# Kernel optimization log

Hardware: AMD Instinct MI355X
Metric: run time of the kernel (lower is better)

The kernel has to match this reference:

```python
import jax, jax.numpy as jnp
import numpy as np

B, N, E = 2, 20000, 160000
D, U = 1, 100          # input_dim, num_units
IN = D + U             # 101
NEG_SLOPE = 0.2        # PyG GATv2Conv default


def setup_inputs() -> dict:
    key = jax.random.key(0)
    ks = jax.random.split(key, 20)
    s = 0.1
    inp = {
        "inputs": jax.random.normal(ks[0], (B, N * D), jnp.float32),
        "state": jax.random.normal(ks[1], (B, N * U), jnp.float32),
        "src": jax.random.randint(ks[2], (E,), 0, N),
        "dst": jax.random.randint(ks[3], (E,), 0, N),
        # GATv2Conv(101, 200) params: lin_l, lin_r, att, out-bias
        "Wl1": jax.random.normal(ks[4], (IN, 2 * U), jnp.float32) * s,
        "bl1": jax.random.normal(ks[5], (2 * U,), jnp.float32) * s,
        "Wr1": jax.random.normal(ks[6], (IN, 2 * U), jnp.float32) * s,
        "br1": jax.random.normal(ks[7], (2 * U,), jnp.float32) * s,
        "att1": jax.random.normal(ks[8], (2 * U,), jnp.float32) * s,
        "bg1": jax.random.normal(ks[9], (2 * U,), jnp.float32) * s,
        "bias0": jax.random.normal(ks[10], (2 * U,), jnp.float32) * s,
        # GATv2Conv(101, 100) params
        "Wl2": jax.random.normal(ks[11], (IN, U), jnp.float32) * s,
        "bl2": jax.random.normal(ks[12], (U,), jnp.float32) * s,
        "Wr2": jax.random.normal(ks[13], (IN, U), jnp.float32) * s,
        "br2": jax.random.normal(ks[14], (U,), jnp.float32) * s,
        "att2": jax.random.normal(ks[15], (U,), jnp.float32) * s,
        "bg2": jax.random.normal(ks[16], (U,), jnp.float32) * s,
        "bias1": jax.random.normal(ks[17], (U,), jnp.float32) * s,
    }
    return inp


def _gatv2(x, src_f, dst_f, Wl, bl, Wr, br, att, bg):
    # x: (B, N, IN); edges (with self-loops) flow src -> dst.
    xl = x @ Wl + bl                                   # (B, N, C) source transform
    xr = x @ Wr + br                                   # (B, N, C) target transform
    msg = jax.nn.leaky_relu(xl[:, src_f] + xr[:, dst_f], NEG_SLOPE)  # (B, Ef, C)
    e = jnp.einsum('bec,c->be', msg, att)              # (B, Ef) attention logits
    seg_max = jax.vmap(lambda v: jax.ops.segment_max(v, dst_f, num_segments=N))(e)
    ea = jnp.exp(e - seg_max[:, dst_f])
    denom = jax.vmap(lambda v: jax.ops.segment_sum(v, dst_f, num_segments=N))(ea)
    alpha = ea / denom[:, dst_f]                       # per-target softmax
    out = jax.vmap(
        lambda a, xs: jax.ops.segment_sum(a[:, None] * xs, dst_f, num_segments=N)
    )(alpha, xl[:, src_f])                             # (B, N, C)
    return out + bg


def reference(inputs, state, src, dst,
              Wl1, bl1, Wr1, br1, att1, bg1, bias0,
              Wl2, bl2, Wr2, br2, att2, bg2, bias1):
    loops = jnp.arange(N)
    src_f = jnp.concatenate([src, loops])              # PyG adds self-loops
    dst_f = jnp.concatenate([dst, loops])
    inputs3 = inputs.reshape(B, N, D)
    state3 = state.reshape(B, N, U)

    # _gc1: GATv2(101 -> 200) + bias_0, sigmoid gates r, u
    xs = jnp.concatenate([inputs3, state3], axis=2)    # (B, N, 101)
    g1 = _gatv2(xs, src_f, dst_f, Wl1, bl1, Wr1, br1, att1, bg1) + bias0
    val = jax.nn.sigmoid(g1)                           # (B, N, 200)
    r = val[..., :U].reshape(B, N * U)
    u = val[..., U:].reshape(B, N * U)

    # _gc2: GATv2(101 -> 100) on [inputs, r*state] + bias_1, tanh
    xs2 = jnp.concatenate([inputs3, (r * state).reshape(B, N, U)], axis=2)
    c = jnp.tanh(_gatv2(xs2, src_f, dst_f, Wl2, bl2, Wr2, br2, att2, bg2) + bias1)
    c = c.reshape(B, N * U)

    new_state = u * state + (1.0 - u) * c              # (B, N*U)
    return new_state
```

## Files before the change

kernel.cpp:

```cpp
#include <hip/hip_runtime.h>
#include <stdint.h>

typedef __attribute__((ext_vector_type(8))) short short8;
typedef __attribute__((ext_vector_type(4))) short short4v;
typedef __attribute__((ext_vector_type(4))) float f32x4;
typedef __attribute__((ext_vector_type(2))) float f32x2;

static constexpr int BB = 2, NN = 20000, UU = 100;
static constexpr int C1 = 200, C2 = 100;
static constexpr int MT = BB * NN;
static constexpr int MPAD = 40064;
static constexpr float NEG = 0.2f;
static constexpr float THR = 20.f;

__device__ __forceinline__ float b2f(short s) {
  union { uint32_t u; float f; } cv; cv.u = ((uint32_t)(uint16_t)s) << 16; return cv.f;
}
__device__ __forceinline__ short f2b(float x) {
  union { float f; uint32_t u; } cv; cv.f = x;
  uint32_t r = cv.u + 0x7FFFu + ((cv.u >> 16) & 1u);
  return (short)(r >> 16);
}
__device__ __forceinline__ int swz(int r, int e) {
  return (((e >> 3) ^ (r & 7)) << 3) + (e & 7);
}
__device__ __forceinline__ int ilv(int m) {
  return (m < NN) ? 2 * m : 2 * (m - NN) + 1;
}

#define GL2LDS(gsrc, ldst)                                                          \
  __builtin_amdgcn_global_load_lds((const __attribute__((address_space(1))) void*)(gsrc), \
                                   (__attribute__((address_space(3))) void*)(ldst), 16, 0, 0)


__global__ void k_zero(int* __restrict__ p, int n) {
  int i = blockIdx.x * 256 + threadIdx.x;
  if (i < n) p[i] = 0;
}

__global__ void k_hist(const int* __restrict__ dst, int E, int* __restrict__ hist) {
  int e = blockIdx.x * 256 + threadIdx.x;
  if (e < E) atomicAdd(&hist[dst[e]], 1);
}

__global__ __launch_bounds__(1024) void k_scan(int* __restrict__ histcur,
                                               int* __restrict__ rowptr, int N, int E) {
  __shared__ int part[1024];
  int t = threadIdx.x;
  int CH = (N + 1023) / 1024;
  int beg = t * CH; if (beg > N) beg = N;
  int end = beg + CH; if (end > N) end = N;
  int s = 0;
  for (int i = beg; i < end; ++i) s += histcur[i];
  part[t] = s;
  __syncthreads();
  for (int off = 1; off < 1024; off <<= 1) {
    int v = (t >= off) ? part[t - off] : 0;
    __syncthreads();
    part[t] += v;
    __syncthreads();
  }
  int base = (t == 0) ? 0 : part[t - 1];
  for (int i = beg; i < end; ++i) {
    int h = histcur[i];
    rowptr[i] = base;
    histcur[i] = base;
    base += h;
  }
  if (t == 1023) rowptr[N] = part[1023];
}

__global__ void k_scatter(const int* __restrict__ src, const int* __restrict__ dst, int E,
                          int* __restrict__ cursor, int* __restrict__ col) {
  int e = blockIdx.x * 256 + threadIdx.x;
  if (e < E) {
    int p = atomicAdd(&cursor[dst[e]], 1);
    col[p] = src[e];
  }
}


__global__ void k_buildA1(const float* __restrict__ inp, const float* __restrict__ st,
                          short* __restrict__ A) {
  int t = blockIdx.x * 256 + threadIdx.x;
  if (t >= MT * 16) return;
  int r = t >> 4, g = t & 15;
  short8 v;
#pragma unroll
  for (int j = 0; j < 8; ++j) {
    int e = g * 8 + j;
    float x = 0.f;
    if (e == 0) x = inp[r];
    else if (e <= 100) x = st[(size_t)r * 100 + e - 1];
    v[j] = f2b(x);
  }
  *(short8*)(A + (size_t)r * 128 + (((g ^ (r & 7)) << 3))) = v;
}

__global__ void k_buildBT(const float* __restrict__ Wl, const float* __restrict__ Wr,
                          short* __restrict__ BT, int SPLIT, int NPAD, int rot) {
  int t = blockIdx.x * 256 + threadIdx.x;
  if (t >= NPAD * 16) return;
  int n = t >> 4, g = t & 15;
  short8 v;
#pragma unroll
  for (int j = 0; j < 8; ++j) {
    int k = g * 8 + j;
    int ksrc = rot ? (k < 100 ? k + 1 : (k == 100 ? 0 : -1)) : (k < 101 ? k : -1);
    float x = 0.f;
    if (ksrc >= 0 && n < 2 * SPLIT)
      x = (n < SPLIT) ? Wl[(size_t)ksrc * SPLIT + n] : Wr[(size_t)ksrc * SPLIT + n - SPLIT];
    v[j] = f2b(x);
  }
  *(short8*)(BT + (size_t)n * 128 + ((g ^ (n & 7)) << 3)) = v;
}

__global__ void k_fillA2(const float* __restrict__ inp, short* __restrict__ A) {
  int r = blockIdx.x * 256 + threadIdx.x;
  if (r >= MT) return;
  short* row = A + (size_t)r * 128;
  row[swz(r, 100)] = f2b(inp[r]);
#pragma unroll
  for (int e = 101; e < 128; ++e) row[swz(r, e)] = 0;
}


template<int NOUT, int SPLIT>
__global__ __launch_bounds__(256) void k_gemm(
    const short* __restrict__ A, const short* __restrict__ BT,
    const float* __restrict__ bias_l, const float* __restrict__ bias_r,
    short* __restrict__ X) {
  __shared__ __align__(16) short As[128 * 128];
  __shared__ __align__(16) short Bs[128 * 128];
  int tid = threadIdx.x;
  int m0 = blockIdx.x * 128;
  int n0 = blockIdx.y * 128;
  {
    const short* gA = A + (size_t)m0 * 128;
    const short* gB = BT + (size_t)n0 * 128;
#pragma unroll
    for (int i = 0; i < 8; ++i) {
      GL2LDS(gA + i * 2048 + tid * 8, As + i * 2048 + tid * 8);
      GL2LDS(gB + i * 2048 + tid * 8, Bs + i * 2048 + tid * 8);
    }
  }
  __syncthreads();

  int wv = tid >> 6, lane = tid & 63;
  int m_off = (wv & 1) * 64, n_off = (wv >> 1) * 64;
  int lrow = lane & 15, lk = lane >> 4;
  f32x4 acc[4][4];
#pragma unroll
  for (int i = 0; i < 4; ++i)
#pragma unroll
    for (int j = 0; j < 4; ++j) acc[i][j] = (f32x4){0.f, 0.f, 0.f, 0.f};

#pragma unroll
  for (int kk = 0; kk < 4; ++kk) {
    int g = kk * 4 + lk;
    short8 a[4], b[4];
#pragma unroll
    for (int f = 0; f < 4; ++f) {
      int ra = m_off + f * 16 + lrow;
      a[f] = *(const short8*)(As + ra * 128 + ((g ^ (ra & 7)) << 3));
      int rb = n_off + f * 16 + lrow;
      b[f] = *(const short8*)(Bs + rb * 128 + ((g ^ (rb & 7)) << 3));
    }
#pragma unroll
    for (int i = 0; i < 4; ++i)
#pragma unroll
      for (int j = 0; j < 4; ++j)
        acc[i][j] = __builtin_amdgcn_mfma_f32_16x16x32_bf16(a[i], b[j], acc[i][j], 0, 0, 0);
  }

#pragma unroll
  for (int j = 0; j < 4; ++j) {
    int n = n0 + n_off + j * 16 + lrow;
    bool nok = n < NOUT;
    float bv = 0.f;
    if (nok) bv = (n < SPLIT) ? bias_l[n] : bias_r[n - SPLIT];
#pragma unroll
    for (int i = 0; i < 4; ++i) {
      int mb = m0 + m_off + i * 16 + lk * 4;
#pragma unroll
      for (int r = 0; r < 4; ++r) {
        int m = mb + r;
        if (nok && m < MT) X[(size_t)ilv(m) * NOUT + n] = f2b(acc[i][j][r] + bv);
      }
    }
  }
}


__global__ __launch_bounds__(256) void k_agg1(
    const short* __restrict__ X1, const int* __restrict__ rowptr, const int* __restrict__ col,
    const float* __restrict__ att, const float* __restrict__ bgv, const float* __restrict__ bias0,
    const float* __restrict__ st, short* __restrict__ A2, float* __restrict__ uu) {
  int w = threadIdx.x >> 6, lane = threadIdx.x & 63;
  int n = blockIdx.x * 4 + w;
  if (n >= NN) return;
  int half = lane >> 5, ll = lane & 31;
  int c0 = (ll < 25 ? ll : 24) * 8;
  int idx = half * NN + n;
  const short* xb = X1 + (size_t)half * 400 + c0;

  float attv[8], xrv[8], num[8];
  {
    f32x4 a0 = (f32x4){0,0,0,0}, a1 = (f32x4){0,0,0,0};
    if (ll < 25) { a0 = *(const f32x4*)(att + c0); a1 = *(const f32x4*)(att + c0 + 4); }
#pragma unroll
    for (int q = 0; q < 4; ++q) { attv[q] = a0[q]; attv[4 + q] = a1[q]; }
    short8 xr8 = *(const short8*)(X1 + (size_t)(2 * n + half) * 400 + 200 + c0);
#pragma unroll
    for (int q = 0; q < 8; ++q) xrv[q] = (ll < 25) ? b2f(xr8[q]) : 0.f;
  }
  float m, denom = 1.f;
  {
    short8 v = *(const short8*)(xb + (size_t)(2 * n) * 400);
    float e = 0.f;
#pragma unroll
    for (int q = 0; q < 8; ++q) {
      float x = b2f(v[q]);
      num[q] = x;
      float msg = x + xrv[q];
      msg = (msg > 0.f) ? msg : NEG * msg;
      e = fmaf(msg, attv[q], e);
    }
#pragma unroll
    for (int off = 16; off > 0; off >>= 1) e += __shfl_xor(e, off);
    m = e;
  }

  int beg = rowptr[n], end = rowptr[n + 1];
  for (int base = beg; base < end; base += 64) {
    int cnt = min(end - base, 64);
    int cv = col[base + (lane < cnt ? lane : 0)];
    int p = 0;
    for (; p + 2 <= cnt; p += 2) {
      int s0 = __shfl(cv, p), s1 = __shfl(cv, p + 1);
      short8 v0 = *(const short8*)(xb + (size_t)(2 * s0) * 400);
      short8 v1 = *(const short8*)(xb + (size_t)(2 * s1) * 400);
      float xs0[8], xs1[8];
      float e0 = 0.f, e1 = 0.f;
#pragma unroll
      for (int q = 0; q < 8; ++q) {
        xs0[q] = b2f(v0[q]);
        float m0_ = xs0[q] + xrv[q]; m0_ = (m0_ > 0.f) ? m0_ : NEG * m0_;
        e0 = fmaf(m0_, attv[q], e0);
        xs1[q] = b2f(v1[q]);
        float m1_ = xs1[q] + xrv[q]; m1_ = (m1_ > 0.f) ? m1_ : NEG * m1_;
        e1 = fmaf(m1_, attv[q], e1);
      }
#pragma unroll
      for (int off = 16; off > 0; off >>= 1) {
        e0 += __shfl_xor(e0, off);
        e1 += __shfl_xor(e1, off);
      }
      float d0 = e0 - m;
      if (d0 > THR) {
        float so = __expf(-d0); denom *= so;
#pragma unroll
        for (int q = 0; q < 8; ++q) num[q] *= so;
        m = e0; d0 = 0.f;
      }
      float pe0 = __expf(d0);
      denom += pe0;
#pragma unroll
      for (int q = 0; q < 8; ++q) num[q] = fmaf(pe0, xs0[q], num[q]);
      float d1 = e1 - m;
      if (d1 > THR) {
        float so = __expf(-d1); denom *= so;
#pragma unroll
        for (int q = 0; q < 8; ++q) num[q] *= so;
        m = e1; d1 = 0.f;
      }
      float pe1 = __expf(d1);
      denom += pe1;
#pragma unroll
      for (int q = 0; q < 8; ++q) num[q] = fmaf(pe1, xs1[q], num[q]);
    }
    if (p < cnt) {
      int s0 = __shfl(cv, p);
      short8 v0 = *(const short8*)(xb + (size_t)(2 * s0) * 400);
      float xs0[8];
      float e0 = 0.f;
#pragma unroll
      for (int q = 0; q < 8; ++q) {
        xs0[q] = b2f(v0[q]);
        float m0_ = xs0[q] + xrv[q]; m0_ = (m0_ > 0.f) ? m0_ : NEG * m0_;
        e0 = fmaf(m0_, attv[q], e0);
      }
#pragma unroll
      for (int off = 16; off > 0; off >>= 1) e0 += __shfl_xor(e0, off);
      float d0 = e0 - m;
      if (d0 > THR) {
        float so = __expf(-d0); denom *= so;
#pragma unroll
        for (int q = 0; q < 8; ++q) num[q] *= so;
        m = e0; d0 = 0.f;
      }
      float pe0 = __expf(d0);
      denom += pe0;
#pragma unroll
      for (int q = 0; q < 8; ++q) num[q] = fmaf(pe0, xs0[q], num[q]);
    }
  }

  float invd = 1.f / denom;
  if (ll < 25) {
    f32x4 g0 = *(const f32x4*)(bgv + c0),   g1 = *(const f32x4*)(bgv + c0 + 4);
    f32x4 h0 = *(const f32x4*)(bias0 + c0), h1 = *(const f32x4*)(bias0 + c0 + 4);
    float vq[8];
#pragma unroll
    for (int q = 0; q < 4; ++q) {
      float o0 = fmaf(num[q], invd, g0[q] + h0[q]);
      vq[q] = 1.f / (1.f + __expf(-o0));
      float o1 = fmaf(num[4 + q], invd, g1[q] + h1[q]);
      vq[4 + q] = 1.f / (1.f + __expf(-o1));
    }
    size_t sb = (size_t)idx * UU;
    if (ll < 12) {
      f32x4 s0 = *(const f32x4*)(st + sb + c0), s1 = *(const f32x4*)(st + sb + c0 + 4);
      short8 wv;
#pragma unroll
      for (int q = 0; q < 4; ++q) { wv[q] = f2b(vq[q] * s0[q]); wv[4 + q] = f2b(vq[4 + q] * s1[q]); }
      *(short8*)(A2 + (size_t)idx * 128 + ((ll ^ (idx & 7)) << 3)) = wv;
    } else if (ll == 12) {
      f32x4 s0 = *(const f32x4*)(st + sb + 96);
      short4v wv;
#pragma unroll
      for (int q = 0; q < 4; ++q) wv[q] = f2b(vq[q] * s0[q]);
      *(short4v*)(A2 + (size_t)idx * 128 + ((12 ^ (idx & 7)) << 3)) = wv;
      *(f32x4*)(uu + sb) = (f32x4){vq[4], vq[5], vq[6], vq[7]};
    } else {
      int uo = c0 - 100;
      *(f32x4*)(uu + sb + uo)     = (f32x4){vq[0], vq[1], vq[2], vq[3]};
      *(f32x4*)(uu + sb + uo + 4) = (f32x4){vq[4], vq[5], vq[6], vq[7]};
    }
  }
}

__global__ __launch_bounds__(256) void k_agg2(
    const short* __restrict__ X2, const int* __restrict__ rowptr, const int* __restrict__ col,
    const float* __restrict__ att, const float* __restrict__ bgv, const float* __restrict__ bias1,
    const float* __restrict__ st, float* __restrict__ out) {
  int w = threadIdx.x >> 6, lane = threadIdx.x & 63;
  int n = blockIdx.x * 4 + w;
  if (n >= NN) return;
  int half = lane >> 5, ll = lane & 31;
  int c0 = (ll < 25 ? ll : 24) * 4;
  int idx = half * NN + n;
  const short* xb = X2 + (size_t)half * 200 + c0;

  float attv[4], xrv[4], num[4];
  {
    f32x4 a0 = (f32x4){0,0,0,0};
    if (ll < 25) a0 = *(const f32x4*)(att + c0);
#pragma unroll
    for (int q = 0; q < 4; ++q) attv[q] = a0[q];
    short4v xr4 = *(const short4v*)(X2 + (size_t)(2 * n + half) * 200 + 100 + c0);
#pragma unroll
    for (int q = 0; q < 4; ++q) xrv[q] = (ll < 25) ? b2f(xr4[q]) : 0.f;
  }
  float m, denom = 1.f;
  {
    short4v v = *(const short4v*)(xb + (size_t)(2 * n) * 200);
    float e = 0.f;
#pragma unroll
    for (int q = 0; q < 4; ++q) {
      float x = b2f(v[q]);
      num[q] = x;
      float msg = x + xrv[q];
      msg = (msg > 0.f) ? msg : NEG * msg;
      e = fmaf(msg, attv[q], e);
    }
#pragma unroll
    for (int off = 16; off > 0; off >>= 1) e += __shfl_xor(e, off);
    m = e;
  }

  int beg = rowptr[n], end = rowptr[n + 1];
  for (int base = beg; base < end; base += 64) {
    int cnt = min(end - base, 64);
    int cv = col[base + (lane < cnt ? lane : 0)];
    int p = 0;
    for (; p + 2 <= cnt; p += 2) {
      int s0 = __shfl(cv, p), s1 = __shfl(cv, p + 1);
      short4v v0 = *(const short4v*)(xb + (size_t)(2 * s0) * 200);
      short4v v1 = *(const short4v*)(xb + (size_t)(2 * s1) * 200);
      float xs0[4], xs1[4];
      float e0 = 0.f, e1 = 0.f;
#pragma unroll
      for (int q = 0; q < 4; ++q) {
        xs0[q] = b2f(v0[q]);
        float m0_ = xs0[q] + xrv[q]; m0_ = (m0_ > 0.f) ? m0_ : NEG * m0_;
        e0 = fmaf(m0_, attv[q], e0);
        xs1[q] = b2f(v1[q]);
        float m1_ = xs1[q] + xrv[q]; m1_ = (m1_ > 0.f) ? m1_ : NEG * m1_;
        e1 = fmaf(m1_, attv[q], e1);
      }
#pragma unroll
      for (int off = 16; off > 0; off >>= 1) {
        e0 += __shfl_xor(e0, off);
        e1 += __shfl_xor(e1, off);
      }
      float d0 = e0 - m;
      if (d0 > THR) {
        float so = __expf(-d0); denom *= so;
#pragma unroll
        for (int q = 0; q < 4; ++q) num[q] *= so;
        m = e0; d0 = 0.f;
      }
      float pe0 = __expf(d0);
      denom += pe0;
#pragma unroll
      for (int q = 0; q < 4; ++q) num[q] = fmaf(pe0, xs0[q], num[q]);
      float d1 = e1 - m;
      if (d1 > THR) {
        float so = __expf(-d1); denom *= so;
#pragma unroll
        for (int q = 0; q < 4; ++q) num[q] *= so;
        m = e1; d1 = 0.f;
      }
      float pe1 = __expf(d1);
      denom += pe1;
#pragma unroll
      for (int q = 0; q < 4; ++q) num[q] = fmaf(pe1, xs1[q], num[q]);
    }
    if (p < cnt) {
      int s0 = __shfl(cv, p);
      short4v v0 = *(const short4v*)(xb + (size_t)(2 * s0) * 200);
      float xs0[4];
      float e0 = 0.f;
#pragma unroll
      for (int q = 0; q < 4; ++q) {
        xs0[q] = b2f(v0[q]);
        float m0_ = xs0[q] + xrv[q]; m0_ = (m0_ > 0.f) ? m0_ : NEG * m0_;
        e0 = fmaf(m0_, attv[q], e0);
      }
#pragma unroll
      for (int off = 16; off > 0; off >>= 1) e0 += __shfl_xor(e0, off);
      float d0 = e0 - m;
      if (d0 > THR) {
        float so = __expf(-d0); denom *= so;
#pragma unroll
        for (int q = 0; q < 4; ++q) num[q] *= so;
        m = e0; d0 = 0.f;
      }
      float pe0 = __expf(d0);
      denom += pe0;
#pragma unroll
      for (int q = 0; q < 4; ++q) num[q] = fmaf(pe0, xs0[q], num[q]);
    }
  }

  float invd = 1.f / denom;
  if (ll < 25) {
    f32x4 g0 = *(const f32x4*)(bgv + c0);
    f32x4 h0 = *(const f32x4*)(bias1 + c0);
    size_t sb = (size_t)idx * UU;
    f32x4 uv = *(const f32x4*)(out + sb + c0);
    f32x4 sv = *(const f32x4*)(st + sb + c0);
    f32x4 res;
#pragma unroll
    for (int q = 0; q < 4; ++q) {
      float o  = fmaf(num[q], invd, g0[q] + h0[q]);
      float cvh = tanhf(o);
      res[q] = uv[q] * sv[q] + (1.f - uv[q]) * cvh;
    }
    *(f32x4*)(out + sb + c0) = res;
  }
}


extern "C" void kernel_launch(void* const* d_in, const int* in_sizes, int n_in,
                              void* d_out, int out_size, void* d_ws, size_t ws_size,
                              hipStream_t stream) {
  const float* inp  = (const float*)d_in[0];
  const float* st   = (const float*)d_in[1];
  const int*   src  = (const int*)d_in[2];
  const int*   dst  = (const int*)d_in[3];
  const float* Wl1  = (const float*)d_in[4];
  const float* bl1  = (const float*)d_in[5];
  const float* Wr1  = (const float*)d_in[6];
  const float* br1  = (const float*)d_in[7];
  const float* att1 = (const float*)d_in[8];
  const float* bg1  = (const float*)d_in[9];
  const float* bias0= (const float*)d_in[10];
  const float* Wl2  = (const float*)d_in[11];
  const float* bl2  = (const float*)d_in[12];
  const float* Wr2  = (const float*)d_in[13];
  const float* br2  = (const float*)d_in[14];
  const float* att2 = (const float*)d_in[15];
  const float* bg2  = (const float*)d_in[16];
  const float* bias1= (const float*)d_in[17];

  const int N = NN;
  const int E = in_sizes[2];

  short* X1  = (short*)d_ws;
  short* X2  = X1;
  short* Aws = X1 + (size_t)MT * 400;
  short* BT1 = Aws + (size_t)MPAD * 128;
  short* BT2 = BT1 + 512 * 128;
  int* rowptr = (int*)(BT2 + 256 * 128);
  int* cursor = rowptr + (N + 1);
  int* col    = cursor + N;

  k_zero<<<(N + 255) / 256, 256, 0, stream>>>(cursor, N);
  k_hist<<<(E + 255) / 256, 256, 0, stream>>>(dst, E, cursor);
  k_scan<<<1, 1024, 0, stream>>>(cursor, rowptr, N, E);
  k_scatter<<<(E + 255) / 256, 256, 0, stream>>>(src, dst, E, cursor, col);

  k_buildA1<<<(MT * 16 + 255) / 256, 256, 0, stream>>>(inp, st, Aws);
  k_buildBT<<<(512 * 16 + 255) / 256, 256, 0, stream>>>(Wl1, Wr1, BT1, C1, 512, 0);
  k_buildBT<<<(256 * 16 + 255) / 256, 256, 0, stream>>>(Wl2, Wr2, BT2, C2, 256, 1);
  {
    dim3 g(MPAD / 128, 4);
    k_gemm<400, 200><<<g, 256, 0, stream>>>(Aws, BT1, bl1, br1, X1);
  }
  k_agg1<<<(NN + 3) / 4, 256, 0, stream>>>(X1, rowptr, col, att1, bg1, bias0, st,
                                           Aws, (float*)d_out);
  k_fillA2<<<(MT + 255) / 256, 256, 0, stream>>>(inp, Aws);
  {
    dim3 g(MPAD / 128, 2);
    k_gemm<200, 100><<<g, 256, 0, stream>>>(Aws, BT2, bl2, br2, X2);
  }
  k_agg2<<<(NN + 3) / 4, 256, 0, stream>>>(X2, rowptr, col, att2, bg2, bias1, st,
                                           (float*)d_out);
}
```

Before: 205.1 us.

## Fuse prep kernels, drop online-max softmax, unroll gathers by four, relayout X

Merges the zeroing, A1 build and both weight-transpose kernels into one prep kernel. The fillA2 kernel is folded into agg1, which now writes the input column and the zero padding itself. The GEMM output layout changes so that both batches' left features for a node sit side by side, ahead of the right features. The aggregation kernels drop the running-max rescaling in the softmax, exponentiating logits directly, and unroll the edge loop to four neighbours for more memory-level parallelism. This saves launches and branches, but relies on the logits being small enough that exp does not overflow.

```diff
diff --git a/kernel.cpp b/kernel.cpp
--- a/kernel.cpp
+++ b/kernel.cpp
@@ -4,14 +4,12 @@
 typedef __attribute__((ext_vector_type(8))) short short8;
 typedef __attribute__((ext_vector_type(4))) short short4v;
 typedef __attribute__((ext_vector_type(4))) float f32x4;
-typedef __attribute__((ext_vector_type(2))) float f32x2;
 
 static constexpr int BB = 2, NN = 20000, UU = 100;
 static constexpr int C1 = 200, C2 = 100;
 static constexpr int MT = BB * NN;
 static constexpr int MPAD = 40064;
 static constexpr float NEG = 0.2f;
-static constexpr float THR = 20.f;
 
 __device__ __forceinline__ float b2f(short s) {
   union { uint32_t u; float f; } cv; cv.u = ((uint32_t)(uint16_t)s) << 16; return cv.f;
@@ -21,22 +19,61 @@
   uint32_t r = cv.u + 0x7FFFu + ((cv.u >> 16) & 1u);
   return (short)(r >> 16);
 }
-__device__ __forceinline__ int swz(int r, int e) {
-  return (((e >> 3) ^ (r & 7)) << 3) + (e & 7);
-}
-__device__ __forceinline__ int ilv(int m) {
-  return (m < NN) ? 2 * m : 2 * (m - NN) + 1;
-}
 
 #define GL2LDS(gsrc, ldst)                                                          \
   __builtin_amdgcn_global_load_lds((const __attribute__((address_space(1))) void*)(gsrc), \
                                    (__attribute__((address_space(3))) void*)(ldst), 16, 0, 0)
 
 
-__global__ void k_zero(int* __restrict__ p, int n) {
-  int i = blockIdx.x * 256 + threadIdx.x;
-  if (i < n) p[i] = 0;
-}
+__global__ void k_prep(const float* __restrict__ inp, const float* __restrict__ st,
+                       const float* __restrict__ Wl1, const float* __restrict__ Wr1,
+                       const float* __restrict__ Wl2, const float* __restrict__ Wr2,
+                       short* __restrict__ A, short* __restrict__ BT1,
+                       short* __restrict__ BT2, int* __restrict__ cursor) {
+  int t = blockIdx.x * 256 + threadIdx.x;
+  if (t < MT * 16) {
+    int r = t >> 4, g = t & 15;
+    short8 v;
+#pragma unroll
+    for (int j = 0; j < 8; ++j) {
+      int e = g * 8 + j;
+      float x = 0.f;
+      if (e == 0) x = inp[r];
+      else if (e <= 100) x = st[(size_t)r * 100 + e - 1];
+      v[j] = f2b(x);
+    }
+    *(short8*)(A + (size_t)r * 128 + ((g ^ (r & 7)) << 3)) = v;
+  }
+  if (t < 512 * 16) {
+    int n = t >> 4, g = t & 15;
+    short8 v;
+#pragma unroll
+    for (int j = 0; j < 8; ++j) {
+      int k = g * 8 + j;
+      float x = 0.f;
+      if (k < 101 && n < 400)
+        x = (n < 200) ? Wl1[(size_t)k * 200 + n] : Wr1[(size_t)k * 200 + n - 200];
+      v[j] = f2b(x);
+    }
+    *(short8*)(BT1 + (size_t)n * 128 + ((g ^ (n & 7)) << 3)) = v;
+  }
+  if (t < 256 * 16) {
+    int n = t >> 4, g = t & 15;
+    short8 v;
+#pragma unroll
+    for (int j = 0; j < 8; ++j) {
+      int k = g * 8 + j;
+      int ksrc = (k < 100) ? k + 1 : ((k == 100) ? 0 : -1);
+      float x = 0.f;
+      if (ksrc >= 0 && n < 200)
+        x = (n < 100) ? Wl2[(size_t)ksrc * 100 + n] : Wr2[(size_t)ksrc * 100 + n - 100];
+      v[j] = f2b(x);
+    }
+    *(short8*)(BT2 + (size_t)n * 128 + ((g ^ (n & 7)) << 3)) = v;
+  }
+  if (t < NN) cursor[t] = 0;
+}
+
 
 __global__ void k_hist(const int* __restrict__ dst, int E, int* __restrict__ hist) {
   int e = blockIdx.x * 256 + threadIdx.x;
@@ -80,51 +117,6 @@
 }
 
 
-__global__ void k_buildA1(const float* __restrict__ inp, const float* __restrict__ st,
-                          short* __restrict__ A) {
-  int t = blockIdx.x * 256 + threadIdx.x;
-  if (t >= MT * 16) return;
-  int r = t >> 4, g = t & 15;
-  short8 v;
-#pragma unroll
-  for (int j = 0; j < 8; ++j) {
-    int e = g * 8 + j;
-    float x = 0.f;
-    if (e == 0) x = inp[r];
-    else if (e <= 100) x = st[(size_t)r * 100 + e - 1];
-    v[j] = f2b(x);
-  }
-  *(short8*)(A + (size_t)r * 128 + (((g ^ (r & 7)) << 3))) = v;
-}
-
-__global__ void k_buildBT(const float* __restrict__ Wl, const float* __restrict__ Wr,
-                          short* __restrict__ BT, int SPLIT, int NPAD, int rot) {
-  int t = blockIdx.x * 256 + threadIdx.x;
-  if (t >= NPAD * 16) return;
-  int n = t >> 4, g = t & 15;
-  short8 v;
-#pragma unroll
-  for (int j = 0; j < 8; ++j) {
-    int k = g * 8 + j;
-    int ksrc = rot ? (k < 100 ? k + 1 : (k == 100 ? 0 : -1)) : (k < 101 ? k : -1);
-    float x = 0.f;
-    if (ksrc >= 0 && n < 2 * SPLIT)
-      x = (n < SPLIT) ? Wl[(size_t)ksrc * SPLIT + n] : Wr[(size_t)ksrc * SPLIT + n - SPLIT];
-    v[j] = f2b(x);
-  }
-  *(short8*)(BT + (size_t)n * 128 + ((g ^ (n & 7)) << 3)) = v;
-}
-
-__global__ void k_fillA2(const float* __restrict__ inp, short* __restrict__ A) {
-  int r = blockIdx.x * 256 + threadIdx.x;
-  if (r >= MT) return;
-  short* row = A + (size_t)r * 128;
-  row[swz(r, 100)] = f2b(inp[r]);
-#pragma unroll
-  for (int e = 101; e < 128; ++e) row[swz(r, e)] = 0;
-}
-
-
 template<int NOUT, int SPLIT>
 __global__ __launch_bounds__(256) void k_gemm(
     const short* __restrict__ A, const short* __restrict__ BT,
@@ -175,17 +167,25 @@
 
 #pragma unroll
   for (int j = 0; j < 4; ++j) {
-    int n = n0 + n_off + j * 16 + lrow;
-    bool nok = n < NOUT;
+    int nc = n0 + n_off + j * 16 + lrow;
+    bool nok = nc < NOUT;
     float bv = 0.f;
-    if (nok) bv = (n < SPLIT) ? bias_l[n] : bias_r[n - SPLIT];
+    int coff = 0;
+    if (nok) {
+      bv   = (nc < SPLIT) ? bias_l[nc] : bias_r[nc - SPLIT];
+      coff = (nc < SPLIT) ? nc : 2 * SPLIT + (nc - SPLIT);
+    }
 #pragma unroll
     for (int i = 0; i < 4; ++i) {
       int mb = m0 + m_off + i * 16 + lk * 4;
 #pragma unroll
       for (int r = 0; r < 4; ++r) {
         int m = mb + r;
-        if (nok && m < MT) X[(size_t)ilv(m) * NOUT + n] = f2b(acc[i][j][r] + bv);
+        if (nok && m < MT) {
+          int b_   = (m >= NN) ? 1 : 0;
+          int node = m - b_ * NN;
+          X[(size_t)node * (4 * SPLIT) + coff + b_ * SPLIT] = f2b(acc[i][j][r] + bv);
+        }
       }
     }
   }
@@ -195,14 +195,15 @@
 __global__ __launch_bounds__(256) void k_agg1(
     const short* __restrict__ X1, const int* __restrict__ rowptr, const int* __restrict__ col,
     const float* __restrict__ att, const float* __restrict__ bgv, const float* __restrict__ bias0,
-    const float* __restrict__ st, short* __restrict__ A2, float* __restrict__ uu) {
+    const float* __restrict__ st, const float* __restrict__ inp,
+    short* __restrict__ A2, float* __restrict__ uu) {
   int w = threadIdx.x >> 6, lane = threadIdx.x & 63;
   int n = blockIdx.x * 4 + w;
   if (n >= NN) return;
   int half = lane >> 5, ll = lane & 31;
   int c0 = (ll < 25 ? ll : 24) * 8;
   int idx = half * NN + n;
-  const short* xb = X1 + (size_t)half * 400 + c0;
+  const short* xb = X1 + (size_t)half * 200 + c0;
 
   float attv[8], xrv[8], num[8];
   {
@@ -210,96 +211,77 @@
     if (ll < 25) { a0 = *(const f32x4*)(att + c0); a1 = *(const f32x4*)(att + c0 + 4); }
 #pragma unroll
     for (int q = 0; q < 4; ++q) { attv[q] = a0[q]; attv[4 + q] = a1[q]; }
-    short8 xr8 = *(const short8*)(X1 + (size_t)(2 * n + half) * 400 + 200 + c0);
+    short8 xr8 = *(const short8*)(X1 + (size_t)n * 800 + 400 + half * 200 + c0);
 #pragma unroll
     for (int q = 0; q < 8; ++q) xrv[q] = (ll < 25) ? b2f(xr8[q]) : 0.f;
   }
-  float m, denom = 1.f;
-  {
-    short8 v = *(const short8*)(xb + (size_t)(2 * n) * 400);
-    float e = 0.f;
+  float denom;
+  {
+    short8 v = *(const short8*)(xb + (size_t)n * 800);
+    float xs[8], e = 0.f;
 #pragma unroll
     for (int q = 0; q < 8; ++q) {
-      float x = b2f(v[q]);
-      num[q] = x;
-      float msg = x + xrv[q];
+      xs[q] = b2f(v[q]);
+      float msg = xs[q] + xrv[q];
       msg = (msg > 0.f) ? msg : NEG * msg;
       e = fmaf(msg, attv[q], e);
     }
 #pragma unroll
     for (int off = 16; off > 0; off >>= 1) e += __shfl_xor(e, off);
-    m = e;
+    float pe = __expf(e);
+    denom = pe;
+#pragma unroll
+    for (int q = 0; q < 8; ++q) num[q] = pe * xs[q];
   }
 
   int beg = rowptr[n], end = rowptr[n + 1];
-  for (int base = beg; base < end; base += 64) {
-    int cnt = min(end - base, 64);
-    int cv = col[base + (lane < cnt ? lane : 0)];
+  for (int bp = beg; bp < end; bp += 64) {
+    int cnt = min(end - bp, 64);
+    int cv = col[bp + (lane < cnt ? lane : 0)];
     int p = 0;
-    for (; p + 2 <= cnt; p += 2) {
+    for (; p + 4 <= cnt; p += 4) {
       int s0 = __shfl(cv, p), s1 = __shfl(cv, p + 1);
-      short8 v0 = *(const short8*)(xb + (size_t)(2 * s0) * 400);
-      short8 v1 = *(const short8*)(xb + (size_t)(2 * s1) * 400);
-      float xs0[8], xs1[8];
-      float e0 = 0.f, e1 = 0.f;
+      int s2 = __shfl(cv, p + 2), s3 = __shfl(cv, p + 3);
+      short8 v0 = *(const short8*)(xb + (size_t)s0 * 800);
+      short8 v1 = *(const short8*)(xb + (size_t)s1 * 800);
+      short8 v2 = *(const short8*)(xb + (size_t)s2 * 800);
+      short8 v3 = *(const short8*)(xb + (size_t)s3 * 800);
+      float xs0[8], xs1[8], xs2[8], xs3[8];
+      float e0 = 0.f, e1 = 0.f, e2 = 0.f, e3 = 0.f;
 #pragma unroll
       for (int q = 0; q < 8; ++q) {
-        xs0[q] = b2f(v0[q]);
-        float m0_ = xs0[q] + xrv[q]; m0_ = (m0_ > 0.f) ? m0_ : NEG * m0_;
-        e0 = fmaf(m0_, attv[q], e0);
-        xs1[q] = b2f(v1[q]);
-        float m1_ = xs1[q] + xrv[q]; m1_ = (m1_ > 0.f) ? m1_ : NEG * m1_;
-        e1 = fmaf(m1_, attv[q], e1);
+        float m_;
+        xs0[q] = b2f(v0[q]); m_ = xs0[q] + xrv[q]; m_ = (m_ > 0.f) ? m_ : NEG * m_; e0 = fmaf(m_, attv[q], e0);
+        xs1[q] = b2f(v1[q]); m_ = xs1[q] + xrv[q]; m_ = (m_ > 0.f) ? m_ : NEG * m_; e1 = fmaf(m_, attv[q], e1);
+        xs2[q] = b2f(v2[q]); m_ = xs2[q] + xrv[q]; m_ = (m_ > 0.f) ? m_ : NEG * m_; e2 = fmaf(m_, attv[q], e2);
+        xs3[q] = b2f(v3[q]); m_ = xs3[q] + xrv[q]; m_ = (m_ > 0.f) ? m_ : NEG * m_; e3 = fmaf(m_, attv[q], e3);
       }
 #pragma unroll
       for (int off = 16; off > 0; off >>= 1) {
         e0 += __shfl_xor(e0, off);
         e1 += __shfl_xor(e1, off);
-      }
-      float d0 = e0 - m;
-      if (d0 > THR) {
-        float so = __expf(-d0); denom *= so;
-#pragma unroll
-        for (int q = 0; q < 8; ++q) num[q] *= so;
-        m = e0; d0 = 0.f;
-      }
-      float pe0 = __expf(d0);
-      denom += pe0;
-#pragma unroll
-      for (int q = 0; q < 8; ++q) num[q] = fmaf(pe0, xs0[q], num[q]);
-      float d1 = e1 - m;
-      if (d1 > THR) {
-        float so = __expf(-d1); denom *= so;
-#pragma unroll
-        for (int q = 0; q < 8; ++q) num[q] *= so;
-        m = e1; d1 = 0.f;
-      }
-      float pe1 = __expf(d1);
-      denom += pe1;
-#pragma unroll
-      for (int q = 0; q < 8; ++q) num[q] = fmaf(pe1, xs1[q], num[q]);
-    }
-    if (p < cnt) {
+        e2 += __shfl_xor(e2, off);
+        e3 += __shfl_xor(e3, off);
+      }
+      float pe0 = __expf(e0), pe1 = __expf(e1), pe2 = __expf(e2), pe3 = __expf(e3);
+      denom += (pe0 + pe1) + (pe2 + pe3);
+#pragma unroll
+      for (int q = 0; q < 8; ++q)
+        num[q] = fmaf(pe3, xs3[q], fmaf(pe2, xs2[q], fmaf(pe1, xs1[q], fmaf(pe0, xs0[q], num[q]))));
+    }
+    for (; p < cnt; ++p) {
       int s0 = __shfl(cv, p);
-      short8 v0 = *(const short8*)(xb + (size_t)(2 * s0) * 400);
-      float xs0[8];
-      float e0 = 0.f;
+      short8 v0 = *(const short8*)(xb + (size_t)s0 * 800);
+      float xs0[8], e0 = 0.f;
 #pragma unroll
       for (int q = 0; q < 8; ++q) {
         xs0[q] = b2f(v0[q]);
-        float m0_ = xs0[q] + xrv[q]; m0_ = (m0_ > 0.f) ? m0_ : NEG * m0_;
-        e0 = fmaf(m0_, attv[q], e0);
+        float m_ = xs0[q] + xrv[q]; m_ = (m_ > 0.f) ? m_ : NEG * m_;
+        e0 = fmaf(m_, attv[q], e0);
       }
 #pragma unroll
       for (int off = 16; off > 0; off >>= 1) e0 += __shfl_xor(e0, off);
-      float d0 = e0 - m;
-      if (d0 > THR) {
-        float so = __expf(-d0); denom *= so;
-#pragma unroll
-        for (int q = 0; q < 8; ++q) num[q] *= so;
-        m = e0; d0 = 0.f;
-      }
-      float pe0 = __expf(d0);
+      float pe0 = __expf(e0);
       denom += pe0;
 #pragma unroll
       for (int q = 0; q < 8; ++q) num[q] = fmaf(pe0, xs0[q], num[q]);
@@ -327,15 +309,20 @@
       *(short8*)(A2 + (size_t)idx * 128 + ((ll ^ (idx & 7)) << 3)) = wv;
     } else if (ll == 12) {
       f32x4 s0 = *(const f32x4*)(st + sb + 96);
-      short4v wv;
+      short8 wv;
 #pragma unroll
       for (int q = 0; q < 4; ++q) wv[q] = f2b(vq[q] * s0[q]);
-      *(short4v*)(A2 + (size_t)idx * 128 + ((12 ^ (idx & 7)) << 3)) = wv;
+      wv[4] = f2b(inp[idx]); wv[5] = 0; wv[6] = 0; wv[7] = 0;
+      *(short8*)(A2 + (size_t)idx * 128 + ((12 ^ (idx & 7)) << 3)) = wv;
       *(f32x4*)(uu + sb) = (f32x4){vq[4], vq[5], vq[6], vq[7]};
     } else {
       int uo = c0 - 100;
       *(f32x4*)(uu + sb + uo)     = (f32x4){vq[0], vq[1], vq[2], vq[3]};
       *(f32x4*)(uu + sb + uo + 4) = (f32x4){vq[4], vq[5], vq[6], vq[7]};
+      if (ll < 16) {
+        short8 z = (short8){0,0,0,0,0,0,0,0};
+        *(short8*)(A2 + (size_t)idx * 128 + ((ll ^ (idx & 7)) << 3)) = z;
+      }
     }
   }
 }
@@ -350,7 +337,7 @@
   int half = lane >> 5, ll = lane & 31;
   int c0 = (ll < 25 ? ll : 24) * 4;
   int idx = half * NN + n;
-  const short* xb = X2 + (size_t)half * 200 + c0;
+  const short* xb = X2 + (size_t)half * 100 + c0;
 
   float attv[4], xrv[4], num[4];
   {
@@ -358,96 +345,77 @@
     if (ll < 25) a0 = *(const f32x4*)(att + c0);
 #pragma unroll
     for (int q = 0; q < 4; ++q) attv[q] = a0[q];
-    short4v xr4 = *(const short4v*)(X2 + (size_t)(2 * n + half) * 200 + 100 + c0);
+    short4v xr4 = *(const short4v*)(X2 + (size_t)n * 400 + 200 + half * 100 + c0);
 #pragma unroll
     for (int q = 0; q < 4; ++q) xrv[q] = (ll < 25) ? b2f(xr4[q]) : 0.f;
   }
-  float m, denom = 1.f;
-  {
-    short4v v = *(const short4v*)(xb + (size_t)(2 * n) * 200);
-    float e = 0.f;
+  float denom;
+  {
+    short4v v = *(const short4v*)(xb + (size_t)n * 400);
+    float xs[4], e = 0.f;
 #pragma unroll
     for (int q = 0; q < 4; ++q) {
-      float x = b2f(v[q]);
-      num[q] = x;
-      float msg = x + xrv[q];
+      xs[q] = b2f(v[q]);
+      float msg = xs[q] + xrv[q];
       msg = (msg > 0.f) ? msg : NEG * msg;
       e = fmaf(msg, attv[q], e);
     }
 #pragma unroll
     for (int off = 16; off > 0; off >>= 1) e += __shfl_xor(e, off);
-    m = e;
+    float pe = __expf(e);
+    denom = pe;
+#pragma unroll
+    for (int q = 0; q < 4; ++q) num[q] = pe * xs[q];
   }
 
   int beg = rowptr[n], end = rowptr[n + 1];
-  for (int base = beg; base < end; base += 64) {
-    int cnt = min(end - base, 64);
-    int cv = col[base + (lane < cnt ? lane : 0)];
+  for (int bp = beg; bp < end; bp += 64) {
+    int cnt = min(end - bp, 64);
+    int cv = col[bp + (lane < cnt ? lane : 0)];
     int p = 0;
-    for (; p + 2 <= cnt; p += 2) {
+    for (; p + 4 <= cnt; p += 4) {
       int s0 = __shfl(cv, p), s1 = __shfl(cv, p + 1);
-      short4v v0 = *(const short4v*)(xb + (size_t)(2 * s0) * 200);
-      short4v v1 = *(const short4v*)(xb + (size_t)(2 * s1) * 200);
-      float xs0[4], xs1[4];
-      float e0 = 0.f, e1 = 0.f;
+      int s2 = __shfl(cv, p + 2), s3 = __shfl(cv, p + 3);
+      short4v v0 = *(const short4v*)(xb + (size_t)s0 * 400);
+      short4v v1 = *(const short4v*)(xb + (size_t)s1 * 400);
+      short4v v2 = *(const short4v*)(xb + (size_t)s2 * 400);
+      short4v v3 = *(const short4v*)(xb + (size_t)s3 * 400);
+      float xs0[4], xs1[4], xs2[4], xs3[4];
+      float e0 = 0.f, e1 = 0.f, e2 = 0.f, e3 = 0.f;
 #pragma unroll
       for (int q = 0; q < 4; ++q) {
-        xs0[q] = b2f(v0[q]);
-        float m0_ = xs0[q] + xrv[q]; m0_ = (m0_ > 0.f) ? m0_ : NEG * m0_;
-        e0 = fmaf(m0_, attv[q], e0);
-        xs1[q] = b2f(v1[q]);
-        float m1_ = xs1[q] + xrv[q]; m1_ = (m1_ > 0.f) ? m1_ : NEG * m1_;
-        e1 = fmaf(m1_, attv[q], e1);
+        float m_;
+        xs0[q] = b2f(v0[q]); m_ = xs0[q] + xrv[q]; m_ = (m_ > 0.f) ? m_ : NEG * m_; e0 = fmaf(m_, attv[q], e0);
+        xs1[q] = b2f(v1[q]); m_ = xs1[q] + xrv[q]; m_ = (m_ > 0.f) ? m_ : NEG * m_; e1 = fmaf(m_, attv[q], e1);
+        xs2[q] = b2f(v2[q]); m_ = xs2[q] + xrv[q]; m_ = (m_ > 0.f) ? m_ : NEG * m_; e2 = fmaf(m_, attv[q], e2);
+        xs3[q] = b2f(v3[q]); m_ = xs3[q] + xrv[q]; m_ = (m_ > 0.f) ? m_ : NEG * m_; e3 = fmaf(m_, attv[q], e3);
       }
 #pragma unroll
       for (int off = 16; off > 0; off >>= 1) {
         e0 += __shfl_xor(e0, off);
         e1 += __shfl_xor(e1, off);
-      }
-      float d0 = e0 - m;
-      if (d0 > THR) {
-        float so = __expf(-d0); denom *= so;
-#pragma unroll
-        for (int q = 0; q < 4; ++q) num[q] *= so;
-        m = e0; d0 = 0.f;
-      }
-      float pe0 = __expf(d0);
-      denom += pe0;
-#pragma unroll
-      for (int q = 0; q < 4; ++q) num[q] = fmaf(pe0, xs0[q], num[q]);
-      float d1 = e1 - m;
-      if (d1 > THR) {
-        float so = __expf(-d1); denom *= so;
-#pragma unroll
-        for (int q = 0; q < 4; ++q) num[q] *= so;
-        m = e1; d1 = 0.f;
-      }
-      float pe1 = __expf(d1);
-      denom += pe1;
-#pragma unroll
-      for (int q = 0; q < 4; ++q) num[q] = fmaf(pe1, xs1[q], num[q]);
-    }
-    if (p < cnt) {
+        e2 += __shfl_xor(e2, off);
+        e3 += __shfl_xor(e3, off);
+      }
+      float pe0 = __expf(e0), pe1 = __expf(e1), pe2 = __expf(e2), pe3 = __expf(e3);
+      denom += (pe0 + pe1) + (pe2 + pe3);
+#pragma unroll
+      for (int q = 0; q < 4; ++q)
+        num[q] = fmaf(pe3, xs3[q], fmaf(pe2, xs2[q], fmaf(pe1, xs1[q], fmaf(pe0, xs0[q], num[q]))));
+    }
+    for (; p < cnt; ++p) {
       int s0 = __shfl(cv, p);
-      short4v v0 = *(const short4v*)(xb + (size_t)(2 * s0) * 200);
-      float xs0[4];
-      float e0 = 0.f;
+      short4v v0 = *(const short4v*)(xb + (size_t)s0 * 400);
+      float xs0[4], e0 = 0.f;
 #pragma unroll
       for (int q = 0; q < 4; ++q) {
         xs0[q] = b2f(v0[q]);
-        float m0_ = xs0[q] + xrv[q]; m0_ = (m0_ > 0.f) ? m0_ : NEG * m0_;
-        e0 = fmaf(m0_, attv[q], e0);
+        float m_ = xs0[q] + xrv[q]; m_ = (m_ > 0.f) ? m_ : NEG * m_;
+        e0 = fmaf(m_, attv[q], e0);
       }
 #pragma unroll
       for (int off = 16; off > 0; off >>= 1) e0 += __shfl_xor(e0, off);
-      float d0 = e0 - m;
-      if (d0 > THR) {
-        float so = __expf(-d0); denom *= so;
-#pragma unroll
-        for (int q = 0; q < 4; ++q) num[q] *= so;
-        m = e0; d0 = 0.f;
-      }
-      float pe0 = __expf(d0);
+      float pe0 = __expf(e0);
       denom += pe0;
 #pragma unroll
       for (int q = 0; q < 4; ++q) num[q] = fmaf(pe0, xs0[q], num[q]);
@@ -464,7 +432,7 @@
     f32x4 res;
 #pragma unroll
     for (int q = 0; q < 4; ++q) {
-      float o  = fmaf(num[q], invd, g0[q] + h0[q]);
+      float o   = fmaf(num[q], invd, g0[q] + h0[q]);
       float cvh = tanhf(o);
       res[q] = uv[q] * sv[q] + (1.f - uv[q]) * cvh;
     }
@@ -500,28 +468,25 @@
 
   short* X1  = (short*)d_ws;
   short* X2  = X1;
-  short* Aws = X1 + (size_t)MT * 400;
+  short* Aws = X1 + (size_t)NN * 800;
   short* BT1 = Aws + (size_t)MPAD * 128;
   short* BT2 = BT1 + 512 * 128;
   int* rowptr = (int*)(BT2 + 256 * 128);
   int* cursor = rowptr + (N + 1);
   int* col    = cursor + N;
 
-  k_zero<<<(N + 255) / 256, 256, 0, stream>>>(cursor, N);
+  k_prep<<<(MT * 16 + 255) / 256, 256, 0, stream>>>(inp, st, Wl1, Wr1, Wl2, Wr2,
+                                                    Aws, BT1, BT2, cursor);
   k_hist<<<(E + 255) / 256, 256, 0, stream>>>(dst, E, cursor);
   k_scan<<<1, 1024, 0, stream>>>(cursor, rowptr, N, E);
   k_scatter<<<(E + 255) / 256, 256, 0, stream>>>(src, dst, E, cursor, col);
 
-  k_buildA1<<<(MT * 16 + 255) / 256, 256, 0, stream>>>(inp, st, Aws);
-  k_buildBT<<<(512 * 16 + 255) / 256, 256, 0, stream>>>(Wl1, Wr1, BT1, C1, 512, 0);
-  k_buildBT<<<(256 * 16 + 255) / 256, 256, 0, stream>>>(Wl2, Wr2, BT2, C2, 256, 1);
   {
     dim3 g(MPAD / 128, 4);
     k_gemm<400, 200><<<g, 256, 0, stream>>>(Aws, BT1, bl1, br1, X1);
   }
-  k_agg1<<<(NN + 3) / 4, 256, 0, stream>>>(X1, rowptr, col, att1, bg1, bias0, st,
+  k_agg1<<<(NN + 3) / 4, 256, 0, stream>>>(X1, rowptr, col, att1, bg1, bias0, st, inp,
                                            Aws, (float*)d_out);
-  k_fillA2<<<(MT + 255) / 256, 256, 0, stream>>>(inp, Aws);
   {
     dim3 g(MPAD / 128, 2);
     k_gemm<200, 100><<<g, 256, 0, stream>>>(Aws, BT2, bl2, br2, X2);
```

Result: faster. 195.4 us (-4.7%).
